# Optimization experiments

Measured on AMD Instinct MI355X. Metric: run time of the kernel, lower is better.

The kernel has to match this reference:

```python
import jax, jax.numpy as jnp
import numpy as np
import math

BATCH, CLS, ATT_DIM, IMG_DIM = 256, 500, 1024, 1024
ATT_HC, HIDDEN_C = 256, 1024
T_TEMP = 10.0
DEGREE = 30
THRESH = math.cos(math.pi * DEGREE / 180.0)
NEG = -9.0e15


def setup_inputs() -> dict:
    key = jax.random.key(0)
    ks = jax.random.split(key, 9)
    inp = {
        "image_feats": jax.random.normal(ks[0], (BATCH, IMG_DIM), dtype=jnp.float32),
        "attributes": jax.random.normal(ks[1], (CLS, ATT_DIM), dtype=jnp.float32),
        "unused": 0,
        # learned parameters (kaiming-like scaling)
        "att_g": jax.random.normal(ks[2], (ATT_DIM, ATT_HC), dtype=jnp.float32) / math.sqrt(ATT_DIM),
        "img_w": jax.random.normal(ks[3], (IMG_DIM, HIDDEN_C), dtype=jnp.float32) / math.sqrt(IMG_DIM),
        "sem_w": jax.random.normal(ks[4], (ATT_DIM, HIDDEN_C), dtype=jnp.float32) / math.sqrt(ATT_DIM),
        "sem_b": jax.random.normal(ks[5], (1, HIDDEN_C), dtype=jnp.float32) / math.sqrt(IMG_DIM),
        "fc_w": jax.random.normal(ks[6], (1, HIDDEN_C), dtype=jnp.float32) / math.sqrt(HIDDEN_C),
        "fc_b": jax.random.normal(ks[7], (1,), dtype=jnp.float32) / math.sqrt(HIDDEN_C),
    }
    return inp


def _get_new_attribute(attributes, att_g):
    # project attributes, cosine similarity between all class pairs
    g = attributes @ att_g                                    # [cls, att_hC]
    gn = g / jnp.linalg.norm(g, axis=1, keepdims=True)        # row-normalize
    sim = gn @ gn.T                                           # [cls, cls] cosine sims
    raw = jnp.where(sim > THRESH, sim, NEG)                   # angular-threshold mask
    attention = jax.nn.softmax(raw * T_TEMP, axis=1)          # [cls, cls]
    return attention @ attributes                             # [cls, att_dim]


def reference(image_feats, attributes, unused, att_g, img_w, sem_w, sem_b, fc_w, fc_b):
    att_outs = _get_new_attribute(attributes, att_g)          # [cls, att_dim]
    # factor the broadcast: identical math to matmul on expanded tensors
    img_h = image_feats @ img_w                               # [batch, hidden]
    sem_h = att_outs @ sem_w                                  # [cls, hidden]
    hidden = jax.nn.relu(img_h[:, None, :] + sem_h[None, :, :] + sem_b[None, :, :])  # [batch, cls, hidden]
    out = jnp.einsum('bch,h->bc', hidden, fc_w[0]) + fc_b[0]  # [batch, cls]
    return out
```

## Files before the change

### kernel.cpp

```cpp
#include <hip/hip_runtime.h>
#include <math.h>

#define BATCH 256
#define CLS 500
#define HIDDEN_ 1024
#define T_TEMP_ 10.0f
#define THRESH_ 0.86602540378443864676f
#define NEGV -9.0e15f

typedef __attribute__((ext_vector_type(8))) short short8;
typedef __attribute__((ext_vector_type(8))) unsigned short u16x8;
typedef __attribute__((ext_vector_type(4))) unsigned short u16x4;
typedef __attribute__((ext_vector_type(4))) float f32x4;
typedef __attribute__((ext_vector_type(2))) float f32x2;

static __device__ __forceinline__ unsigned short f2bf(float x) {
    unsigned int u = __builtin_bit_cast(unsigned int, x);
    u += 0x7fff + ((u >> 16) & 1);
    return (unsigned short)(u >> 16);
}
static __device__ __forceinline__ float bf2f(unsigned short v) {
    return __builtin_bit_cast(float, (unsigned int)v << 16);
}
static __device__ __forceinline__ u16x8 pack8(const float4& a, const float4& b) {
    u16x8 o;
    o[0] = f2bf(a.x); o[1] = f2bf(a.y); o[2] = f2bf(a.z); o[3] = f2bf(a.w);
    o[4] = f2bf(b.x); o[5] = f2bf(b.y); o[6] = f2bf(b.z); o[7] = f2bf(b.w);
    return o;
}

__global__ __launch_bounds__(256) void convert_kernel(
    const float* __restrict__ attrs, const float* __restrict__ imgf,
    const float* __restrict__ attg, const float* __restrict__ imgw,
    const float* __restrict__ semw,
    unsigned short* __restrict__ attrs_bf, unsigned short* __restrict__ imgf_bf,
    unsigned short* __restrict__ attgT, unsigned short* __restrict__ imgwT,
    unsigned short* __restrict__ semwT)
{
    __shared__ unsigned short tb[64][72];
    const int t = threadIdx.x;
    int bid = blockIdx.x;

    if (bid < 378) {
        const float* s; unsigned short* d; int idx;
        if (bid < 250) { s = attrs; d = attrs_bf; idx = bid * 2048 + t * 8; }
        else           { s = imgf;  d = imgf_bf;  idx = (bid - 250) * 2048 + t * 8; }
        float4 v0 = *(const float4*)&s[idx];
        float4 v1 = *(const float4*)&s[idx + 4];
        *(u16x8*)&d[idx] = pack8(v0, v1);
        return;
    }
    bid -= 378;
    const float* s; unsigned short* d; int Csz;
    if (bid < 64)       { s = attg; d = attgT; Csz = 256; }
    else if (bid < 320) { bid -= 64;  s = imgw; d = imgwT; Csz = 1024; }
    else                { bid -= 320; s = semw; d = semwT; Csz = 1024; }
    const int tiles_c = Csz >> 6;
    const int tr = bid / tiles_c, tc = bid % tiles_c;
    {
        const int r = t >> 2, cq = (t & 3) * 16;
        const float* p = &s[(size_t)(tr * 64 + r) * Csz + tc * 64 + cq];
        float4 v0 = *(const float4*)(p);
        float4 v1 = *(const float4*)(p + 4);
        float4 v2 = *(const float4*)(p + 8);
        float4 v3 = *(const float4*)(p + 12);
        *(u16x8*)&tb[r][cq]     = pack8(v0, v1);
        *(u16x8*)&tb[r][cq + 8] = pack8(v2, v3);
    }
    __syncthreads();
    {
        const int c = t >> 2, r0 = (t & 3) * 16;
        u16x8 o0, o1;
        #pragma unroll
        for (int i = 0; i < 8; ++i) { o0[i] = tb[r0 + i][c]; o1[i] = tb[r0 + 8 + i][c]; }
        unsigned short* q = &d[(size_t)(tc * 64 + c) * 1024 + tr * 64 + r0];
        *(u16x8*)q = o0;
        *(u16x8*)(q + 8) = o1;
    }
}

__global__ __launch_bounds__(256) void mfma_gemm_bf(
    const unsigned short* __restrict__ A1, int alim1,
    const unsigned short* __restrict__ A2, int a2t0, int alim2,
    const unsigned short* __restrict__ B1, const unsigned short* __restrict__ B2,
    float* __restrict__ C, unsigned short* __restrict__ Cbf,
    int M, int N, int K, int klen)
{
    __shared__ unsigned short As[64][40];
    __shared__ unsigned short Bs[128][40];

    const int t  = threadIdx.x;
    const int bx = blockIdx.x;
    const int n0 = blockIdx.y * 128;
    const int k0 = blockIdx.z * klen;

    const unsigned short* A; const unsigned short* B; int ar0, alim;
    if (bx < a2t0) { A = A1; B = B1; ar0 = bx * 64;          alim = alim1; }
    else           { A = A2; B = B2; ar0 = (bx - a2t0) * 64; alim = alim2; }

    const int w = t >> 6, lane = t & 63;
    const int wr = w >> 1, wc = w & 1;
    const int fr = lane & 15, kg = lane >> 4;

    const int a_row = t >> 2, a_k = (t & 3) * 8;
    const int b_row = t >> 1, b_k = (t & 1) * 16;
    const int gra = ar0 + a_row;
    const int grb = n0 + b_row;
    const bool va = gra < alim;
    const bool vb = grb < N;
    const size_t abase = (size_t)gra * K + a_k;
    const size_t bbase = (size_t)grb * K + b_k;

    u16x8 zz = {0,0,0,0,0,0,0,0};
    u16x8 pa = zz, pb0 = zz, pb1 = zz;
    if (va) pa = *(const u16x8*)&A[abase + k0];
    if (vb) { pb0 = *(const u16x8*)&B[bbase + k0]; pb1 = *(const u16x8*)&B[bbase + k0 + 8]; }

    f32x4 zero4 = {0.f, 0.f, 0.f, 0.f};
    f32x4 acc[2][4];
    #pragma unroll
    for (int i = 0; i < 2; ++i)
        #pragma unroll
        for (int j = 0; j < 4; ++j) acc[i][j] = zero4;

    for (int kb = k0; kb < k0 + klen; kb += 32) {
        *(u16x8*)&As[a_row][a_k] = pa;
        *(u16x8*)&Bs[b_row][b_k] = pb0;
        *(u16x8*)&Bs[b_row][b_k + 8] = pb1;
        __syncthreads();

        const int kn = kb + 32;
        if (kn < k0 + klen) {
            if (va) pa = *(const u16x8*)&A[abase + kn];
            if (vb) { pb0 = *(const u16x8*)&B[bbase + kn]; pb1 = *(const u16x8*)&B[bbase + kn + 8]; }
        }

        short8 af[2], bfr[4];
        #pragma unroll
        for (int i = 0; i < 2; ++i)
            af[i] = *(short8*)&As[wr * 32 + i * 16 + fr][kg * 8];
        #pragma unroll
        for (int j = 0; j < 4; ++j)
            bfr[j] = *(short8*)&Bs[wc * 64 + j * 16 + fr][kg * 8];
        #pragma unroll
        for (int i = 0; i < 2; ++i)
            #pragma unroll
            for (int j = 0; j < 4; ++j)
                acc[i][j] = __builtin_amdgcn_mfma_f32_16x16x32_bf16(
                    af[i], bfr[j], acc[i][j], 0, 0, 0);
        __syncthreads();
    }

    const int orow0 = bx * 64 + wr * 32, ocol0 = n0 + wc * 64;
    if (Cbf) {
        unsigned short* Cw = Cbf + (size_t)blockIdx.z * M * N;
        #pragma unroll
        for (int i = 0; i < 2; ++i) {
            const int r0 = orow0 + i * 16 + kg * 4;
            #pragma unroll
            for (int j = 0; j < 4; ++j) {
                const int cc = ocol0 + j * 16 + fr;
                if (cc >= N) continue;
                #pragma unroll
                for (int r = 0; r < 4; ++r) {
                    const int rr = r0 + r;
                    if (rr < M) Cw[(size_t)rr * N + cc] = f2bf(acc[i][j][r]);
                }
            }
        }
    } else {
        float* Cw = C + (gridDim.z > 1 ? (size_t)blockIdx.z * M * N : 0);
        #pragma unroll
        for (int i = 0; i < 2; ++i) {
            const int r0 = orow0 + i * 16 + kg * 4;
            #pragma unroll
            for (int j = 0; j < 4; ++j) {
                const int cc = ocol0 + j * 16 + fr;
                if (cc >= N) continue;
                #pragma unroll
                for (int r = 0; r < 4; ++r) {
                    const int rr = r0 + r;
                    if (rr < M) Cw[(size_t)rr * N + cc] = acc[i][j][r];
                }
            }
        }
    }
}

__global__ __launch_bounds__(256) void reduce_norm_kernel(
    const float* __restrict__ part, unsigned short* __restrict__ gn_bf)
{
    const int c = blockIdx.x, t = threadIdx.x;
    float v = 0.f;
    #pragma unroll
    for (int z = 0; z < 8; ++z) v += part[(size_t)z * (CLS * 256) + c * 256 + t];
    float ss = v * v;
    #pragma unroll
    for (int off = 32; off >= 1; off >>= 1) ss += __shfl_down(ss, off);
    __shared__ float red[4];
    const int wave = t >> 6, lane = t & 63;
    if (lane == 0) red[wave] = ss;
    __syncthreads();
    const float tot = red[0] + red[1] + red[2] + red[3];
    const float rn  = 1.f / sqrtf(tot);
    gn_bf[c * 256 + t] = f2bf(v * rn);
}

__global__ __launch_bounds__(256) void softmax_att_kernel(
    const float* __restrict__ sim, const float* __restrict__ attrs,
    unsigned short* __restrict__ att_outs)
{
    const int c = blockIdx.x, t = threadIdx.x;
    __shared__ float p_s[512];
    __shared__ float redm[4];
    __shared__ float reds[4];

    const float d0 = sim[(size_t)c * CLS + t];
    const float d1 = (t + 256 < CLS) ? sim[(size_t)c * CLS + t + 256] : NEGV;

    float vmax = fmaxf((d0 > THRESH_) ? d0 : NEGV, (d1 > THRESH_) ? d1 : NEGV);
    #pragma unroll
    for (int off = 32; off >= 1; off >>= 1) vmax = fmaxf(vmax, __shfl_down(vmax, off));
    const int wave = t >> 6, lane = t & 63;
    if (lane == 0) redm[wave] = vmax;
    __syncthreads();
    const float m = fmaxf(fmaxf(redm[0], redm[1]), fmaxf(redm[2], redm[3]));

    const float p0 = (d0 > THRESH_) ? expf(T_TEMP_ * (d0 - m)) : 0.f;
    const float p1 = (d1 > THRESH_) ? expf(T_TEMP_ * (d1 - m)) : 0.f;
    p_s[t] = p0;
    p_s[t + 256] = p1;
    float vsum = p0 + p1;
    #pragma unroll
    for (int off = 32; off >= 1; off >>= 1) vsum += __shfl_down(vsum, off);
    if (lane == 0) reds[wave] = vsum;
    __syncthreads();
    const float inv = 1.f / (reds[0] + reds[1] + reds[2] + reds[3]);

    float acc[4] = {0.f, 0.f, 0.f, 0.f};
    for (int base = 0; base < 512; base += 64) {
        const float pv_l = p_s[base + lane];
        unsigned long long mask = __ballot(pv_l > 0.f);
        while (mask) {
            const int l = __ffsll((long long)mask) - 1;
            mask &= mask - 1;
            const int c2 = base + l;
            const float pv = p_s[c2];
            const float* ar = &attrs[(size_t)c2 * 1024 + t];
            #pragma unroll
            for (int j = 0; j < 4; ++j) acc[j] += pv * ar[256 * j];
        }
    }
    #pragma unroll
    for (int j = 0; j < 4; ++j)
        att_outs[(size_t)c * 1024 + t + 256 * j] = f2bf(acc[j] * inv);
}

__global__ __launch_bounds__(256) void fused_out_partial(
    const unsigned short* __restrict__ part, int ks, const float* __restrict__ sem_b,
    const float* __restrict__ fc_w, float* __restrict__ outpart, int h_per)
{
    __shared__ float imgs[64][68];
    __shared__ float sems[64][68];
    __shared__ float fcs[128];

    const size_t pstride = (size_t)756 * 1024;
    const int t  = threadIdx.x;
    const int tb = t >> 4, tc = t & 15;
    const int b0 = blockIdx.x * 64, c0 = blockIdx.y * 64;
    const int h0 = blockIdx.z * h_per;

    if (t < (h_per >> 2)) *(float4*)&fcs[t * 4] = *(const float4*)&fc_w[h0 + t * 4];

    f32x2 acc2[4][4];
    #pragma unroll
    for (int i = 0; i < 4; ++i)
        #pragma unroll
        for (int j = 0; j < 4; ++j) acc2[i][j] = (f32x2){0.f, 0.f};

    for (int hs = 0; hs < (h_per >> 6); ++hs) {
        const int hb = h0 + hs * 64;
        #pragma unroll
        for (int i = 0; i < 4; ++i) {
            const int row = (t >> 4) + 16 * i;
            const int col = (t & 15) * 4;
            f32x4 iv = {0.f, 0.f, 0.f, 0.f};
            const unsigned short* pi = &part[(size_t)(b0 + row) * 1024 + hb + col];
            for (int z = 0; z < ks; ++z) {
                u16x4 vz = *(const u16x4*)(pi + (size_t)z * pstride);
                iv[0] += bf2f(vz[0]); iv[1] += bf2f(vz[1]);
                iv[2] += bf2f(vz[2]); iv[3] += bf2f(vz[3]);
            }
            *(f32x4*)&imgs[row][col] = iv;

            f32x4 sv = {0.f, 0.f, 0.f, 0.f};
            if (c0 + row < CLS) {
                const unsigned short* ps = &part[(size_t)(256 + c0 + row) * 1024 + hb + col];
                for (int z = 0; z < ks; ++z) {
                    u16x4 vz = *(const u16x4*)(ps + (size_t)z * pstride);
                    sv[0] += bf2f(vz[0]); sv[1] += bf2f(vz[1]);
                    sv[2] += bf2f(vz[2]); sv[3] += bf2f(vz[3]);
                }
                float4 bb = *(const float4*)&sem_b[hb + col];
                sv[0] += bb.x; sv[1] += bb.y; sv[2] += bb.z; sv[3] += bb.w;
            }
            *(f32x4*)&sems[row][col] = sv;
        }
        __syncthreads();

        #pragma unroll
        for (int h4 = 0; h4 < 16; ++h4) {
            float4 ia[4], sa[4];
            #pragma unroll
            for (int i = 0; i < 4; ++i) ia[i] = *(float4*)&imgs[tb + 16 * i][h4 * 4];
            #pragma unroll
            for (int j = 0; j < 4; ++j) sa[j] = *(float4*)&sems[tc + 16 * j][h4 * 4];
            const float4 wv = *(const float4*)&fcs[hs * 64 + h4 * 4];
            #pragma unroll
            for (int e2 = 0; e2 < 2; ++e2) {
                const f32x2 w2 = {(&wv.x)[2 * e2], (&wv.x)[2 * e2 + 1]};
                f32x2 ia2[4], sa2[4];
                #pragma unroll
                for (int i = 0; i < 4; ++i)
                    ia2[i] = (f32x2){(&ia[i].x)[2 * e2], (&ia[i].x)[2 * e2 + 1]};
                #pragma unroll
                for (int j = 0; j < 4; ++j)
                    sa2[j] = (f32x2){(&sa[j].x)[2 * e2], (&sa[j].x)[2 * e2 + 1]};
                #pragma unroll
                for (int i = 0; i < 4; ++i)
                    #pragma unroll
                    for (int j = 0; j < 4; ++j) {
                        f32x2 s = ia2[i] + sa2[j];
                        s = __builtin_elementwise_max(s, (f32x2){0.f, 0.f});
                        acc2[i][j] += s * w2;
                    }
            }
        }
        __syncthreads();
    }

    const int nh = blockIdx.z;
    #pragma unroll
    for (int i = 0; i < 4; ++i) {
        const int b = b0 + tb + 16 * i;
        #pragma unroll
        for (int j = 0; j < 4; ++j) {
            const int cc = c0 + tc + 16 * j;
            if (cc < CLS)
                outpart[((size_t)nh * BATCH + b) * CLS + cc] = acc2[i][j][0] + acc2[i][j][1];
        }
    }
}

__global__ __launch_bounds__(256) void finalize_kernel(
    const float* __restrict__ partial, const float* __restrict__ fc_b,
    float* __restrict__ out, int nsplit)
{
    const int idx = blockIdx.x * 256 + threadIdx.x;
    if (idx >= BATCH * CLS) return;
    float s = fc_b[0];
    for (int nh = 0; nh < nsplit; ++nh)
        s += partial[(size_t)nh * BATCH * CLS + idx];
    out[idx] = s;
}

extern "C" void kernel_launch(void* const* d_in, const int* in_sizes, int n_in,
                              void* d_out, int out_size, void* d_ws, size_t ws_size,
                              hipStream_t stream)
{
    const float* image_feats = (const float*)d_in[0];
    const float* attributes  = (const float*)d_in[1];
    const float* att_g       = (const float*)d_in[3];
    const float* img_w       = (const float*)d_in[4];
    const float* sem_w       = (const float*)d_in[5];
    const float* sem_b       = (const float*)d_in[6];
    const float* fc_w        = (const float*)d_in[7];
    const float* fc_b        = (const float*)d_in[8];
    float* out = (float*)d_out;

    char* ws = (char*)d_ws;
    size_t off = 0;
    auto alloc = [&](size_t b) { size_t o = off; off = (off + b + 255) & ~(size_t)255; return o; };
    const size_t o_attr = alloc((size_t)500 * 1024 * 2);
    const size_t o_imgf = alloc((size_t)256 * 1024 * 2);
    const size_t o_attg = alloc((size_t)256 * 1024 * 2);
    const size_t o_imgw = alloc((size_t)1024 * 1024 * 2);
    const size_t o_semw = alloc((size_t)1024 * 1024 * 2);
    const size_t o_gn   = alloc((size_t)500 * 256 * 2);
    const size_t o_atto = alloc((size_t)500 * 1024 * 2);
    const size_t o_gp   = alloc((size_t)8 * 500 * 256 * 4);
    const size_t base   = off;

    int ks = 4, nh = 16;
    while (base + (size_t)ks * 756 * 1024 * 2 + (size_t)nh * BATCH * CLS * 4 + 512 > ws_size) {
        if (ks > 1) ks >>= 1;
        else if (nh > 8) nh = 8;
        else break;
    }
    const size_t o_hidp = alloc((size_t)ks * 756 * 1024 * 2);
    const size_t o_outp = alloc((size_t)nh * BATCH * CLS * 4);
    (void)o_outp;

    unsigned short* attr_bf = (unsigned short*)(ws + o_attr);
    unsigned short* imgf_bf = (unsigned short*)(ws + o_imgf);
    unsigned short* attgT   = (unsigned short*)(ws + o_attg);
    unsigned short* imgwT   = (unsigned short*)(ws + o_imgw);
    unsigned short* semwT   = (unsigned short*)(ws + o_semw);
    unsigned short* gn_bf   = (unsigned short*)(ws + o_gn);
    unsigned short* atto_bf = (unsigned short*)(ws + o_atto);
    float* gpart_sim        = (float*)(ws + o_gp);
    unsigned short* hidP    = (unsigned short*)(ws + o_hidp);
    float* outP             = (float*)(ws + o_outp);

    convert_kernel<<<954, 256, 0, stream>>>(
        attributes, image_feats, att_g, img_w, sem_w,
        attr_bf, imgf_bf, attgT, imgwT, semwT);

    mfma_gemm_bf<<<dim3(8, 2, 8), 256, 0, stream>>>(
        attr_bf, 500, attr_bf, 1000, 500, attgT, attgT,
        gpart_sim, nullptr, CLS, 256, 1024, 128);

    reduce_norm_kernel<<<CLS, 256, 0, stream>>>(gpart_sim, gn_bf);

    mfma_gemm_bf<<<dim3(8, 4, 1), 256, 0, stream>>>(
        gn_bf, 500, gn_bf, 1000, 500, gn_bf, gn_bf,
        gpart_sim, nullptr, CLS, CLS, 256, 256);

    softmax_att_kernel<<<CLS, 256, 0, stream>>>(gpart_sim, attributes, atto_bf);

    mfma_gemm_bf<<<dim3(12, 8, ks), 256, 0, stream>>>(
        imgf_bf, 256, atto_bf, 4, 500, imgwT, semwT,
        nullptr, hidP, 756, 1024, 1024, 1024 / ks);

    fused_out_partial<<<dim3(BATCH / 64, (CLS + 63) / 64, nh), 256, 0, stream>>>(
        hidP, ks, sem_b, fc_w, outP, HIDDEN_ / nh);

    finalize_kernel<<<(BATCH * CLS + 255) / 256, 256, 0, stream>>>(outP, fc_b, out, nh);
}
```

Before: 66.07 us.

## Fuse bf16 conversion into GEMMs and merge reductions via atomic block counters

Drops the separate fp32-to-bf16 conversion/transpose kernel: the attribute projection and the hidden GEMMs now load fp32 inputs and weights directly, converting and transposing into shared memory. The row-norm reduction is folded into the projection GEMM, and the final split-sum plus bias is folded into the output kernel. Both folds use per-group atomic counters with spin-waits, which assume all blocks in a group are co-resident. The hidden GEMM now uses a fixed 2-way K split and the output kernel a fixed 8-way hidden split, and a memset to clear the counters is added. This removes kernel launches and intermediate buffer round-trips, but the GEMMs repeat the fp32 conversion work and read twice as many bytes per weight load.

```diff
diff --git a/kernel.cpp b/kernel.cpp
--- a/kernel.cpp
+++ b/kernel.cpp
@@ -3,7 +3,6 @@
 
 #define BATCH 256
 #define CLS 500
-#define HIDDEN_ 1024
 #define T_TEMP_ 10.0f
 #define THRESH_ 0.86602540378443864676f
 #define NEGV -9.0e15f
@@ -22,6 +21,7 @@
 static __device__ __forceinline__ float bf2f(unsigned short v) {
     return __builtin_bit_cast(float, (unsigned int)v << 16);
 }
+static __device__ __forceinline__ float fel(const float4& v, int j) { return (&v.x)[j]; }
 static __device__ __forceinline__ u16x8 pack8(const float4& a, const float4& b) {
     u16x8 o;
     o[0] = f2bf(a.x); o[1] = f2bf(a.y); o[2] = f2bf(a.z); o[3] = f2bf(a.w);
@@ -29,53 +29,113 @@
     return o;
 }
 
-__global__ __launch_bounds__(256) void convert_kernel(
-    const float* __restrict__ attrs, const float* __restrict__ imgf,
-    const float* __restrict__ attg, const float* __restrict__ imgw,
-    const float* __restrict__ semw,
-    unsigned short* __restrict__ attrs_bf, unsigned short* __restrict__ imgf_bf,
-    unsigned short* __restrict__ attgT, unsigned short* __restrict__ imgwT,
-    unsigned short* __restrict__ semwT)
+__global__ __launch_bounds__(256) void g_norm_kernel(
+    const float* __restrict__ attrs, const float* __restrict__ attg,
+    float* __restrict__ gpart, unsigned short* __restrict__ gn_bf,
+    unsigned int* __restrict__ cnt)
 {
-    __shared__ unsigned short tb[64][72];
+    __shared__ unsigned short As[64][40];
+    __shared__ unsigned short Bs[128][40];
+    __shared__ float red[4];
+    __shared__ unsigned int rank_s;
     const int t = threadIdx.x;
-    int bid = blockIdx.x;
-
-    if (bid < 378) {
-        const float* s; unsigned short* d; int idx;
-        if (bid < 250) { s = attrs; d = attrs_bf; idx = bid * 2048 + t * 8; }
-        else           { s = imgf;  d = imgf_bf;  idx = (bid - 250) * 2048 + t * 8; }
-        float4 v0 = *(const float4*)&s[idx];
-        float4 v1 = *(const float4*)&s[idx + 4];
-        *(u16x8*)&d[idx] = pack8(v0, v1);
-        return;
-    }
-    bid -= 378;
-    const float* s; unsigned short* d; int Csz;
-    if (bid < 64)       { s = attg; d = attgT; Csz = 256; }
-    else if (bid < 320) { bid -= 64;  s = imgw; d = imgwT; Csz = 1024; }
-    else                { bid -= 320; s = semw; d = semwT; Csz = 1024; }
-    const int tiles_c = Csz >> 6;
-    const int tr = bid / tiles_c, tc = bid % tiles_c;
-    {
-        const int r = t >> 2, cq = (t & 3) * 16;
-        const float* p = &s[(size_t)(tr * 64 + r) * Csz + tc * 64 + cq];
-        float4 v0 = *(const float4*)(p);
-        float4 v1 = *(const float4*)(p + 4);
-        float4 v2 = *(const float4*)(p + 8);
-        float4 v3 = *(const float4*)(p + 12);
-        *(u16x8*)&tb[r][cq]     = pack8(v0, v1);
-        *(u16x8*)&tb[r][cq + 8] = pack8(v2, v3);
-    }
+    const int bid = blockIdx.x;
+    const int mt = bid >> 4, nt = (bid >> 3) & 1, split = bid & 7;
+    const int n0 = nt * 128, ar0 = mt * 64, k0 = split * 128;
+
+    const int w = t >> 6, lane = t & 63;
+    const int wr = w >> 1, wc = w & 1;
+    const int fr = lane & 15, kg = lane >> 4;
+    const int as_row = t >> 2, as_kq = t & 3;
+    const int bs_nc = (t & 31) * 4, bs_kr = t >> 5;
+
+    f32x4 acc[2][4];
+    #pragma unroll
+    for (int i = 0; i < 2; ++i)
+        #pragma unroll
+        for (int j = 0; j < 4; ++j) acc[i][j] = (f32x4){0.f, 0.f, 0.f, 0.f};
+
+    for (int kb = k0; kb < k0 + 128; kb += 32) {
+        {
+            const int gr = ar0 + as_row;
+            float4 v0 = make_float4(0.f,0.f,0.f,0.f), v1 = v0;
+            if (gr < CLS) {
+                const float* ap = &attrs[(size_t)gr * 1024 + kb + as_kq * 8];
+                v0 = *(const float4*)ap; v1 = *(const float4*)(ap + 4);
+            }
+            *(u16x8*)&As[as_row][as_kq * 8] = pack8(v0, v1);
+        }
+        {
+            const float* bp = &attg[(size_t)(kb + bs_kr * 4) * 256 + n0 + bs_nc];
+            float4 r0 = *(const float4*)(bp);
+            float4 r1 = *(const float4*)(bp + 256);
+            float4 r2 = *(const float4*)(bp + 512);
+            float4 r3 = *(const float4*)(bp + 768);
+            #pragma unroll
+            for (int j = 0; j < 4; ++j) {
+                unsigned int lo = (unsigned int)f2bf(fel(r0, j)) | ((unsigned int)f2bf(fel(r1, j)) << 16);
+                unsigned int hi = (unsigned int)f2bf(fel(r2, j)) | ((unsigned int)f2bf(fel(r3, j)) << 16);
+                uint2 u2; u2.x = lo; u2.y = hi;
+                *(uint2*)&Bs[bs_nc + j][bs_kr * 4] = u2;
+            }
+        }
+        __syncthreads();
+        short8 af[2], bfr[4];
+        #pragma unroll
+        for (int i = 0; i < 2; ++i) af[i] = *(short8*)&As[wr * 32 + i * 16 + fr][kg * 8];
+        #pragma unroll
+        for (int j = 0; j < 4; ++j) bfr[j] = *(short8*)&Bs[wc * 64 + j * 16 + fr][kg * 8];
+        #pragma unroll
+        for (int i = 0; i < 2; ++i)
+            #pragma unroll
+            for (int j = 0; j < 4; ++j)
+                acc[i][j] = __builtin_amdgcn_mfma_f32_16x16x32_bf16(af[i], bfr[j], acc[i][j], 0, 0, 0);
+        __syncthreads();
+    }
+
+    float* Gp = gpart + (size_t)split * (512 * 256);
+    const int orow0 = ar0 + wr * 32, ocol0 = n0 + wc * 64;
+    #pragma unroll
+    for (int i = 0; i < 2; ++i) {
+        const int r0 = orow0 + i * 16 + kg * 4;
+        #pragma unroll
+        for (int j = 0; j < 4; ++j) {
+            const int cc = ocol0 + j * 16 + fr;
+            #pragma unroll
+            for (int r = 0; r < 4; ++r)
+                __hip_atomic_store(&Gp[(size_t)(r0 + r) * 256 + cc], acc[i][j][r],
+                                   __ATOMIC_RELAXED, __HIP_MEMORY_SCOPE_AGENT);
+        }
+    }
+    asm volatile("s_waitcnt vmcnt(0)" ::: "memory");
     __syncthreads();
-    {
-        const int c = t >> 2, r0 = (t & 3) * 16;
-        u16x8 o0, o1;
-        #pragma unroll
-        for (int i = 0; i < 8; ++i) { o0[i] = tb[r0 + i][c]; o1[i] = tb[r0 + 8 + i][c]; }
-        unsigned short* q = &d[(size_t)(tc * 64 + c) * 1024 + tr * 64 + r0];
-        *(u16x8*)q = o0;
-        *(u16x8*)(q + 8) = o1;
+    if (t == 0) {
+        rank_s = __hip_atomic_fetch_add(&cnt[mt * 32], 1u, __ATOMIC_RELAXED,
+                                        __HIP_MEMORY_SCOPE_AGENT);
+        while (__hip_atomic_load(&cnt[mt * 32], __ATOMIC_RELAXED,
+                                 __HIP_MEMORY_SCOPE_AGENT) < 16u)
+            __builtin_amdgcn_s_sleep(1);
+    }
+    __syncthreads();
+    const int rank = (int)rank_s;
+
+    #pragma unroll
+    for (int rr4 = 0; rr4 < 4; ++rr4) {
+        const int r = mt * 64 + rank * 4 + rr4;
+        if (r < CLS) {
+            float v = 0.f;
+            #pragma unroll
+            for (int z = 0; z < 8; ++z)
+                v += gpart[(size_t)z * (512 * 256) + (size_t)r * 256 + t];
+            float ss = v * v;
+            #pragma unroll
+            for (int off = 32; off >= 1; off >>= 1) ss += __shfl_down(ss, off);
+            if (lane == 0) red[w] = ss;
+            __syncthreads();
+            const float tot = red[0] + red[1] + red[2] + red[3];
+            gn_bf[r * 256 + t] = f2bf(v * (1.f / sqrtf(tot)));
+            __syncthreads();
+        }
     }
 }
 
@@ -113,15 +173,14 @@
 
     u16x8 zz = {0,0,0,0,0,0,0,0};
     u16x8 pa = zz, pb0 = zz, pb1 = zz;
-    if (va) pa = *(const u16x8*)&A[abase + k0];
-    if (vb) { pb0 = *(const u16x8*)&B[bbase + k0]; pb1 = *(const u16x8*)&B[bbase + k0 + 8]; }
-
-    f32x4 zero4 = {0.f, 0.f, 0.f, 0.f};
+    if (va) pa = *(const u16x8*)&A1[abase + k0];
+    if (vb) { pb0 = *(const u16x8*)&B1[bbase + k0]; pb1 = *(const u16x8*)&B1[bbase + k0 + 8]; }
+
     f32x4 acc[2][4];
     #pragma unroll
     for (int i = 0; i < 2; ++i)
         #pragma unroll
-        for (int j = 0; j < 4; ++j) acc[i][j] = zero4;
+        for (int j = 0; j < 4; ++j) acc[i][j] = (f32x4){0.f, 0.f, 0.f, 0.f};
 
     for (int kb = k0; kb < k0 + klen; kb += 32) {
         *(u16x8*)&As[a_row][a_k] = pa;
@@ -137,17 +196,14 @@
 
         short8 af[2], bfr[4];
         #pragma unroll
+        for (int i = 0; i < 2; ++i) af[i] = *(short8*)&As[wr * 32 + i * 16 + fr][kg * 8];
+        #pragma unroll
+        for (int j = 0; j < 4; ++j) bfr[j] = *(short8*)&Bs[wc * 64 + j * 16 + fr][kg * 8];
+        #pragma unroll
         for (int i = 0; i < 2; ++i)
-            af[i] = *(short8*)&As[wr * 32 + i * 16 + fr][kg * 8];
-        #pragma unroll
-        for (int j = 0; j < 4; ++j)
-            bfr[j] = *(short8*)&Bs[wc * 64 + j * 16 + fr][kg * 8];
-        #pragma unroll
-        for (int i = 0; i < 2; ++i)
             #pragma unroll
             for (int j = 0; j < 4; ++j)
-                acc[i][j] = __builtin_amdgcn_mfma_f32_16x16x32_bf16(
-                    af[i], bfr[j], acc[i][j], 0, 0, 0);
+                acc[i][j] = __builtin_amdgcn_mfma_f32_16x16x32_bf16(af[i], bfr[j], acc[i][j], 0, 0, 0);
         __syncthreads();
     }
 
@@ -185,25 +241,6 @@
             }
         }
     }
-}
-
-__global__ __launch_bounds__(256) void reduce_norm_kernel(
-    const float* __restrict__ part, unsigned short* __restrict__ gn_bf)
-{
-    const int c = blockIdx.x, t = threadIdx.x;
-    float v = 0.f;
-    #pragma unroll
-    for (int z = 0; z < 8; ++z) v += part[(size_t)z * (CLS * 256) + c * 256 + t];
-    float ss = v * v;
-    #pragma unroll
-    for (int off = 32; off >= 1; off >>= 1) ss += __shfl_down(ss, off);
-    __shared__ float red[4];
-    const int wave = t >> 6, lane = t & 63;
-    if (lane == 0) red[wave] = ss;
-    __syncthreads();
-    const float tot = red[0] + red[1] + red[2] + red[3];
-    const float rn  = 1.f / sqrtf(tot);
-    gn_bf[c * 256 + t] = f2bf(v * rn);
 }
 
 __global__ __launch_bounds__(256) void softmax_att_kernel(
@@ -256,21 +293,112 @@
         att_outs[(size_t)c * 1024 + t + 256 * j] = f2bf(acc[j] * inv);
 }
 
-__global__ __launch_bounds__(256) void fused_out_partial(
-    const unsigned short* __restrict__ part, int ks, const float* __restrict__ sem_b,
-    const float* __restrict__ fc_w, float* __restrict__ outpart, int h_per)
+__global__ __launch_bounds__(256) void hid_kernel(
+    const float* __restrict__ imgf, const unsigned short* __restrict__ atto_bf,
+    const float* __restrict__ imgw, const float* __restrict__ semw,
+    unsigned short* __restrict__ hidP)
+{
+    __shared__ unsigned short As[64][40];
+    __shared__ unsigned short Bs[128][40];
+    const int t = threadIdx.x;
+    const int mt = blockIdx.x, nt = blockIdx.y, split = blockIdx.z;
+    const int n0 = nt * 128, k0 = split * 512;
+    const bool img_side = (mt < 4);
+    const int ar0 = img_side ? mt * 64 : (mt - 4) * 64;
+    const int alim = img_side ? 256 : 500;
+    const float* Bf = img_side ? imgw : semw;
+
+    const int w = t >> 6, lane = t & 63;
+    const int wr = w >> 1, wc = w & 1;
+    const int fr = lane & 15, kg = lane >> 4;
+    const int as_row = t >> 2, as_kq = t & 3;
+    const int bs_nc = (t & 31) * 4, bs_kr = t >> 5;
+
+    f32x4 acc[2][4];
+    #pragma unroll
+    for (int i = 0; i < 2; ++i)
+        #pragma unroll
+        for (int j = 0; j < 4; ++j) acc[i][j] = (f32x4){0.f, 0.f, 0.f, 0.f};
+
+    for (int kb = k0; kb < k0 + 512; kb += 32) {
+        {
+            const int gr = ar0 + as_row;
+            if (img_side) {
+                float4 v0 = make_float4(0.f,0.f,0.f,0.f), v1 = v0;
+                if (gr < alim) {
+                    const float* ap = &imgf[(size_t)gr * 1024 + kb + as_kq * 8];
+                    v0 = *(const float4*)ap; v1 = *(const float4*)(ap + 4);
+                }
+                *(u16x8*)&As[as_row][as_kq * 8] = pack8(v0, v1);
+            } else {
+                u16x8 pa = {0,0,0,0,0,0,0,0};
+                if (gr < alim) pa = *(const u16x8*)&atto_bf[(size_t)gr * 1024 + kb + as_kq * 8];
+                *(u16x8*)&As[as_row][as_kq * 8] = pa;
+            }
+        }
+        {
+            const float* bp = &Bf[(size_t)(kb + bs_kr * 4) * 1024 + n0 + bs_nc];
+            float4 r0 = *(const float4*)(bp);
+            float4 r1 = *(const float4*)(bp + 1024);
+            float4 r2 = *(const float4*)(bp + 2048);
+            float4 r3 = *(const float4*)(bp + 3072);
+            #pragma unroll
+            for (int j = 0; j < 4; ++j) {
+                unsigned int lo = (unsigned int)f2bf(fel(r0, j)) | ((unsigned int)f2bf(fel(r1, j)) << 16);
+                unsigned int hi = (unsigned int)f2bf(fel(r2, j)) | ((unsigned int)f2bf(fel(r3, j)) << 16);
+                uint2 u2; u2.x = lo; u2.y = hi;
+                *(uint2*)&Bs[bs_nc + j][bs_kr * 4] = u2;
+            }
+        }
+        __syncthreads();
+        short8 af[2], bfr[4];
+        #pragma unroll
+        for (int i = 0; i < 2; ++i) af[i] = *(short8*)&As[wr * 32 + i * 16 + fr][kg * 8];
+        #pragma unroll
+        for (int j = 0; j < 4; ++j) bfr[j] = *(short8*)&Bs[wc * 64 + j * 16 + fr][kg * 8];
+        #pragma unroll
+        for (int i = 0; i < 2; ++i)
+            #pragma unroll
+            for (int j = 0; j < 4; ++j)
+                acc[i][j] = __builtin_amdgcn_mfma_f32_16x16x32_bf16(af[i], bfr[j], acc[i][j], 0, 0, 0);
+        __syncthreads();
+    }
+
+    unsigned short* Cw = hidP + (size_t)split * (756 * 1024);
+    const int orow0 = mt * 64 + wr * 32, ocol0 = n0 + wc * 64;
+    #pragma unroll
+    for (int i = 0; i < 2; ++i) {
+        const int r0 = orow0 + i * 16 + kg * 4;
+        #pragma unroll
+        for (int j = 0; j < 4; ++j) {
+            const int cc = ocol0 + j * 16 + fr;
+            #pragma unroll
+            for (int r = 0; r < 4; ++r) {
+                const int rr = r0 + r;
+                if (rr < 756) Cw[(size_t)rr * 1024 + cc] = f2bf(acc[i][j][r]);
+            }
+        }
+    }
+}
+
+__global__ __launch_bounds__(256) void fused_kernel(
+    const unsigned short* __restrict__ part, const float* __restrict__ sem_b,
+    const float* __restrict__ fc_w, const float* __restrict__ fc_b,
+    float* __restrict__ outP, float* __restrict__ out,
+    unsigned int* __restrict__ cnt)
 {
     __shared__ float imgs[64][68];
     __shared__ float sems[64][68];
     __shared__ float fcs[128];
-
+    __shared__ unsigned int rank_s;
     const size_t pstride = (size_t)756 * 1024;
-    const int t  = threadIdx.x;
+    const int t = threadIdx.x;
+    const int bid = blockIdx.x;
+    const int bx = bid & 3, by = (bid >> 2) & 7, bz = bid >> 5;
+    const int b0 = bx * 64, c0 = by * 64, h0 = bz * 128;
     const int tb = t >> 4, tc = t & 15;
-    const int b0 = blockIdx.x * 64, c0 = blockIdx.y * 64;
-    const int h0 = blockIdx.z * h_per;
-
-    if (t < (h_per >> 2)) *(float4*)&fcs[t * 4] = *(const float4*)&fc_w[h0 + t * 4];
+
+    if (t < 32) *(float4*)&fcs[t * 4] = *(const float4*)&fc_w[h0 + t * 4];
 
     f32x2 acc2[4][4];
     #pragma unroll
@@ -278,7 +406,7 @@
         #pragma unroll
         for (int j = 0; j < 4; ++j) acc2[i][j] = (f32x2){0.f, 0.f};
 
-    for (int hs = 0; hs < (h_per >> 6); ++hs) {
+    for (int hs = 0; hs < 2; ++hs) {
         const int hb = h0 + hs * 64;
         #pragma unroll
         for (int i = 0; i < 4; ++i) {
@@ -286,7 +414,8 @@
             const int col = (t & 15) * 4;
             f32x4 iv = {0.f, 0.f, 0.f, 0.f};
             const unsigned short* pi = &part[(size_t)(b0 + row) * 1024 + hb + col];
-            for (int z = 0; z < ks; ++z) {
+            #pragma unroll
+            for (int z = 0; z < 2; ++z) {
                 u16x4 vz = *(const u16x4*)(pi + (size_t)z * pstride);
                 iv[0] += bf2f(vz[0]); iv[1] += bf2f(vz[1]);
                 iv[2] += bf2f(vz[2]); iv[3] += bf2f(vz[3]);
@@ -295,14 +424,15 @@
 
             f32x4 sv = {0.f, 0.f, 0.f, 0.f};
             if (c0 + row < CLS) {
-                const unsigned short* ps = &part[(size_t)(256 + c0 + row) * 1024 + hb + col];
-                for (int z = 0; z < ks; ++z) {
-                    u16x4 vz = *(const u16x4*)(ps + (size_t)z * pstride);
+                const unsigned short* ps2 = &part[(size_t)(256 + c0 + row) * 1024 + hb + col];
+                #pragma unroll
+                for (int z = 0; z < 2; ++z) {
+                    u16x4 vz = *(const u16x4*)(ps2 + (size_t)z * pstride);
                     sv[0] += bf2f(vz[0]); sv[1] += bf2f(vz[1]);
                     sv[2] += bf2f(vz[2]); sv[3] += bf2f(vz[3]);
                 }
-                float4 bb = *(const float4*)&sem_b[hb + col];
-                sv[0] += bb.x; sv[1] += bb.y; sv[2] += bb.z; sv[3] += bb.w;
+                const f32x4 bb = *(const f32x4*)&sem_b[hb + col];
+                sv += bb;
             }
             *(f32x4*)&sems[row][col] = sv;
         }
@@ -310,22 +440,20 @@
 
         #pragma unroll
         for (int h4 = 0; h4 < 16; ++h4) {
-            float4 ia[4], sa[4];
-            #pragma unroll
-            for (int i = 0; i < 4; ++i) ia[i] = *(float4*)&imgs[tb + 16 * i][h4 * 4];
-            #pragma unroll
-            for (int j = 0; j < 4; ++j) sa[j] = *(float4*)&sems[tc + 16 * j][h4 * 4];
-            const float4 wv = *(const float4*)&fcs[hs * 64 + h4 * 4];
+            f32x4 ia[4], sa[4];
+            #pragma unroll
+            for (int i = 0; i < 4; ++i) ia[i] = *(f32x4*)&imgs[tb + 16 * i][h4 * 4];
+            #pragma unroll
+            for (int j = 0; j < 4; ++j) sa[j] = *(f32x4*)&sems[tc + 16 * j][h4 * 4];
+            const f32x4 wv = *(const f32x4*)&fcs[hs * 64 + h4 * 4];
             #pragma unroll
             for (int e2 = 0; e2 < 2; ++e2) {
-                const f32x2 w2 = {(&wv.x)[2 * e2], (&wv.x)[2 * e2 + 1]};
+                const f32x2 w2 = {wv[2 * e2], wv[2 * e2 + 1]};
                 f32x2 ia2[4], sa2[4];
                 #pragma unroll
-                for (int i = 0; i < 4; ++i)
-                    ia2[i] = (f32x2){(&ia[i].x)[2 * e2], (&ia[i].x)[2 * e2 + 1]};
+                for (int i = 0; i < 4; ++i) ia2[i] = (f32x2){ia[i][2 * e2], ia[i][2 * e2 + 1]};
                 #pragma unroll
-                for (int j = 0; j < 4; ++j)
-                    sa2[j] = (f32x2){(&sa[j].x)[2 * e2], (&sa[j].x)[2 * e2 + 1]};
+                for (int j = 0; j < 4; ++j) sa2[j] = (f32x2){sa[j][2 * e2], sa[j][2 * e2 + 1]};
                 #pragma unroll
                 for (int i = 0; i < 4; ++i)
                     #pragma unroll
@@ -339,7 +467,6 @@
         __syncthreads();
     }
 
-    const int nh = blockIdx.z;
     #pragma unroll
     for (int i = 0; i < 4; ++i) {
         const int b = b0 + tb + 16 * i;
@@ -347,93 +474,75 @@
         for (int j = 0; j < 4; ++j) {
             const int cc = c0 + tc + 16 * j;
             if (cc < CLS)
-                outpart[((size_t)nh * BATCH + b) * CLS + cc] = acc2[i][j][0] + acc2[i][j][1];
-        }
-    }
-}
-
-__global__ __launch_bounds__(256) void finalize_kernel(
-    const float* __restrict__ partial, const float* __restrict__ fc_b,
-    float* __restrict__ out, int nsplit)
-{
-    const int idx = blockIdx.x * 256 + threadIdx.x;
-    if (idx >= BATCH * CLS) return;
-    float s = fc_b[0];
-    for (int nh = 0; nh < nsplit; ++nh)
-        s += partial[(size_t)nh * BATCH * CLS + idx];
-    out[idx] = s;
+                __hip_atomic_store(&outP[((size_t)bz * BATCH + b) * CLS + cc],
+                                   acc2[i][j][0] + acc2[i][j][1],
+                                   __ATOMIC_RELAXED, __HIP_MEMORY_SCOPE_AGENT);
+        }
+    }
+    asm volatile("s_waitcnt vmcnt(0)" ::: "memory");
+    __syncthreads();
+    const int g = bid & 31;
+    if (t == 0) {
+        rank_s = __hip_atomic_fetch_add(&cnt[g * 32], 1u, __ATOMIC_RELAXED,
+                                        __HIP_MEMORY_SCOPE_AGENT);
+        while (__hip_atomic_load(&cnt[g * 32], __ATOMIC_RELAXED,
+                                 __HIP_MEMORY_SCOPE_AGENT) < 8u)
+            __builtin_amdgcn_s_sleep(1);
+    }
+    __syncthreads();
+    const int rank = (int)rank_s;
+    const float bias = fc_b[0];
+    #pragma unroll
+    for (int pass = 0; pass < 2; ++pass) {
+        const int row = b0 + rank * 8 + pass * 4 + (t >> 6);
+        const int col = c0 + (t & 63);
+        if (col < CLS) {
+            float s = bias;
+            #pragma unroll
+            for (int z = 0; z < 8; ++z)
+                s += outP[((size_t)z * BATCH + row) * CLS + col];
+            out[(size_t)row * CLS + col] = s;
+        }
+    }
 }
 
 extern "C" void kernel_launch(void* const* d_in, const int* in_sizes, int n_in,
                               void* d_out, int out_size, void* d_ws, size_t ws_size,
                               hipStream_t stream)
 {
-    const float* image_feats = (const float*)d_in[0];
-    const float* attributes  = (const float*)d_in[1];
-    const float* att_g       = (const float*)d_in[3];
-    const float* img_w       = (const float*)d_in[4];
-    const float* sem_w       = (const float*)d_in[5];
-    const float* sem_b       = (const float*)d_in[6];
-    const float* fc_w        = (const float*)d_in[7];
-    const float* fc_b        = (const float*)d_in[8];
+    const float* imgf  = (const float*)d_in[0];
+    const float* attrs = (const float*)d_in[1];
+    const float* attg  = (const float*)d_in[3];
+    const float* imgw  = (const float*)d_in[4];
+    const float* semw  = (const float*)d_in[5];
+    const float* semb  = (const float*)d_in[6];
+    const float* fcw   = (const float*)d_in[7];
+    const float* fcb   = (const float*)d_in[8];
     float* out = (float*)d_out;
 
     char* ws = (char*)d_ws;
-    size_t off = 0;
+    size_t off = 8192;
     auto alloc = [&](size_t b) { size_t o = off; off = (off + b + 255) & ~(size_t)255; return o; };
-    const size_t o_attr = alloc((size_t)500 * 1024 * 2);
-    const size_t o_imgf = alloc((size_t)256 * 1024 * 2);
-    const size_t o_attg = alloc((size_t)256 * 1024 * 2);
-    const size_t o_imgw = alloc((size_t)1024 * 1024 * 2);
-    const size_t o_semw = alloc((size_t)1024 * 1024 * 2);
-    const size_t o_gn   = alloc((size_t)500 * 256 * 2);
-    const size_t o_atto = alloc((size_t)500 * 1024 * 2);
-    const size_t o_gp   = alloc((size_t)8 * 500 * 256 * 4);
-    const size_t base   = off;
-
-    int ks = 4, nh = 16;
-    while (base + (size_t)ks * 756 * 1024 * 2 + (size_t)nh * BATCH * CLS * 4 + 512 > ws_size) {
-        if (ks > 1) ks >>= 1;
-        else if (nh > 8) nh = 8;
-        else break;
-    }
-    const size_t o_hidp = alloc((size_t)ks * 756 * 1024 * 2);
-    const size_t o_outp = alloc((size_t)nh * BATCH * CLS * 4);
-    (void)o_outp;
-
-    unsigned short* attr_bf = (unsigned short*)(ws + o_attr);
-    unsigned short* imgf_bf = (unsigned short*)(ws + o_imgf);
-    unsigned short* attgT   = (unsigned short*)(ws + o_attg);
-    unsigned short* imgwT   = (unsigned short*)(ws + o_imgw);
-    unsigned short* semwT   = (unsigned short*)(ws + o_semw);
-    unsigned short* gn_bf   = (unsigned short*)(ws + o_gn);
-    unsigned short* atto_bf = (unsigned short*)(ws + o_atto);
-    float* gpart_sim        = (float*)(ws + o_gp);
-    unsigned short* hidP    = (unsigned short*)(ws + o_hidp);
-    float* outP             = (float*)(ws + o_outp);
-
-    convert_kernel<<<954, 256, 0, stream>>>(
-        attributes, image_feats, att_g, img_w, sem_w,
-        attr_bf, imgf_bf, attgT, imgwT, semwT);
-
-    mfma_gemm_bf<<<dim3(8, 2, 8), 256, 0, stream>>>(
-        attr_bf, 500, attr_bf, 1000, 500, attgT, attgT,
-        gpart_sim, nullptr, CLS, 256, 1024, 128);
-
-    reduce_norm_kernel<<<CLS, 256, 0, stream>>>(gpart_sim, gn_bf);
+    unsigned int* cnt1 = (unsigned int*)ws;
+    unsigned int* cnt2 = (unsigned int*)(ws + 4096);
+    float* gpart          = (float*)(ws + alloc((size_t)8 * 512 * 256 * 4));
+    unsigned short* gn_bf = (unsigned short*)(ws + alloc((size_t)500 * 256 * 2));
+    float* sim            = (float*)(ws + alloc((size_t)CLS * CLS * 4));
+    unsigned short* atto  = (unsigned short*)(ws + alloc((size_t)500 * 1024 * 2));
+    unsigned short* hidP  = (unsigned short*)(ws + alloc((size_t)2 * 756 * 1024 * 2));
+    float* outP           = (float*)(ws + alloc((size_t)8 * BATCH * CLS * 4));
+
+    hipMemsetAsync(d_ws, 0, 8192, stream);
+
+    g_norm_kernel<<<128, 256, 0, stream>>>(attrs, attg, gpart, gn_bf, cnt1);
 
     mfma_gemm_bf<<<dim3(8, 4, 1), 256, 0, stream>>>(
         gn_bf, 500, gn_bf, 1000, 500, gn_bf, gn_bf,
-        gpart_sim, nullptr, CLS, CLS, 256, 256);
-
-    softmax_att_kernel<<<CLS, 256, 0, stream>>>(gpart_sim, attributes, atto_bf);
-
-    mfma_gemm_bf<<<dim3(12, 8, ks), 256, 0, stream>>>(
-        imgf_bf, 256, atto_bf, 4, 500, imgwT, semwT,
-        nullptr, hidP, 756, 1024, 1024, 1024 / ks);
-
-    fused_out_partial<<<dim3(BATCH / 64, (CLS + 63) / 64, nh), 256, 0, stream>>>(
-        hidP, ks, sem_b, fc_w, outP, HIDDEN_ / nh);
-
-    finalize_kernel<<<(BATCH * CLS + 255) / 256, 256, 0, stream>>>(outP, fc_b, out, nh);
-}
+        sim, nullptr, 500, 500, 256, 256);
+
+    softmax_att_kernel<<<CLS, 256, 0, stream>>>(sim, attrs, atto);
+
+    hid_kernel<<<dim3(12, 8, 2), 256, 0, stream>>>(imgf, atto, imgw, semw, hidP);
+
+    fused_kernel<<<256, 256, 0, stream>>>(hidP, semb, fcw, fcb, outP, out, cnt2);
+}
```

After: 74.80 us. 13.2% more time.
